# Optimization experiments

Hardware: AMD Instinct MI355X
Metric: run time of the kernel (lower is better)

Reference implementation:

```python
import jax, jax.numpy as jnp
import numpy as np

D_MODEL, NHEAD, INT_DIM = 1024, 16, 4096
HEAD_DIM = D_MODEL // NHEAD
EPS = 1e-5


def _layernorm(x, gamma, beta):
    mu = jnp.mean(x, axis=-1, keepdims=True)
    var = jnp.var(x, axis=-1, keepdims=True)
    return (x - mu) * jax.lax.rsqrt(var + EPS) * gamma + beta


def setup_inputs() -> dict:
    key = jax.random.key(0)
    ks = jax.random.split(key, 16)
    B, T = 2, 2048
    s = 0.02
    inp = {
        'x': jax.random.normal(ks[0], (B, T, D_MODEL), dtype=jnp.float32),
        'Wq': jax.random.normal(ks[1], (D_MODEL, D_MODEL), dtype=jnp.float32) * s,
        'bq': jnp.zeros((D_MODEL,), jnp.float32),
        'Wk': jax.random.normal(ks[2], (D_MODEL, D_MODEL), dtype=jnp.float32) * s,
        'bk': jnp.zeros((D_MODEL,), jnp.float32),
        'Wv': jax.random.normal(ks[3], (D_MODEL, D_MODEL), dtype=jnp.float32) * s,
        'bv': jnp.zeros((D_MODEL,), jnp.float32),
        'Wo': jax.random.normal(ks[4], (D_MODEL, D_MODEL), dtype=jnp.float32) * s,
        'bo': jnp.zeros((D_MODEL,), jnp.float32),
        'ln1_g': jnp.ones((D_MODEL,), jnp.float32),
        'ln1_b': jnp.zeros((D_MODEL,), jnp.float32),
        'ln2_g': jnp.ones((D_MODEL,), jnp.float32),
        'ln2_b': jnp.zeros((D_MODEL,), jnp.float32),
        'W1': jax.random.normal(ks[5], (D_MODEL, INT_DIM), dtype=jnp.float32) * s,
        'b1': jnp.zeros((INT_DIM,), jnp.float32),
        'W2': jax.random.normal(ks[6], (INT_DIM, D_MODEL), dtype=jnp.float32) * s,
        'b2': jnp.zeros((D_MODEL,), jnp.float32),
    }
    return inp


def reference(x, Wq, bq, Wk, bk, Wv, bv, Wo, bo, ln1_g, ln1_b, ln2_g, ln2_b, W1, b1, W2, b2):
    B, T, D = x.shape
    # projections
    q = (x @ Wq + bq).reshape(B, T, NHEAD, HEAD_DIM).transpose(0, 2, 1, 3)
    k = (x @ Wk + bk).reshape(B, T, NHEAD, HEAD_DIM).transpose(0, 2, 1, 3)
    v = (x @ Wv + bv).reshape(B, T, NHEAD, HEAD_DIM).transpose(0, 2, 1, 3)
    # attention: [B,H,T,T] scores, softmax over keys
    scores = jnp.einsum('bhqd,bhkd->bhqk', q, k) / jnp.sqrt(jnp.float32(HEAD_DIM))
    attn = jax.nn.softmax(scores, axis=-1)
    out = jnp.einsum('bhqk,bhkd->bhqd', attn, v)
    out = out.transpose(0, 2, 1, 3).reshape(B, T, D)
    attn_output = out @ Wo + bo
    # residual + layernorm 1
    h = _layernorm(x + attn_output, ln1_g, ln1_b)
    # FFN
    ff = jax.nn.relu(h @ W1 + b1) @ W2 + b2
    # residual + layernorm 2
    return _layernorm(h + ff, ln2_g, ln2_b)
```

## Files before the change

### kernel.cpp

```cpp
#include <hip/hip_runtime.h>
#include <cstdint>

#define DEVI __device__ __forceinline__

typedef float f32x4 __attribute__((ext_vector_type(4)));
typedef __bf16 bf16x8 __attribute__((ext_vector_type(8)));
typedef unsigned int u32x4v __attribute__((ext_vector_type(4)));
typedef unsigned short u16;
typedef unsigned int u32;
typedef unsigned long long u64;

#define LOG2E 1.44269504088896f
#define QSCALE (0.125f * LOG2E)

DEVI u16 bf16bits(float f) {
    u32 u = __builtin_bit_cast(u32, f);
    u32 r = u + 0x7fffu + ((u >> 16) & 1u);
    return (u16)(r >> 16);
}

DEVI u32 pack2bf(float a, float b) {
    u16 x = __builtin_bit_cast(u16, (__bf16)a);
    u16 y = __builtin_bit_cast(u16, (__bf16)b);
    return (u32)x | ((u32)y << 16);
}

DEVI float ex2(float x) {
    float r;
    asm("v_exp_f32 %0, %1" : "=v"(r) : "v"(x));
    return r;
}

DEVI void gload16(const void* g, const void* l) {
    __builtin_amdgcn_global_load_lds(
        (const __attribute__((address_space(1))) void*)(u64)(uintptr_t)g,
        (__attribute__((address_space(3))) void*)(u32)(uintptr_t)l,
        16, 0, 0);
}

#define VMCNT0_BARRIER()                                   \
    asm volatile("s_waitcnt vmcnt(0)" ::: "memory");       \
    __builtin_amdgcn_s_barrier()

__global__ __launch_bounds__(256)
void prep_kernel(const float* __restrict__ x, u16* __restrict__ xb,
                 const float* __restrict__ Wq, const float* __restrict__ Wk,
                 const float* __restrict__ Wv, const float* __restrict__ Wo,
                 u16* __restrict__ Wqt, u16* __restrict__ Wkt,
                 u16* __restrict__ Wvt, u16* __restrict__ Wot,
                 const float* __restrict__ W1, u16* __restrict__ W1t,
                 const float* __restrict__ W2, u16* __restrict__ W2t) {
    __shared__ float t[64][65];
    const int b = blockIdx.x;
    const int tid = threadIdx.x;
    if (b < 4096) {
        int i = b * 256 + tid;
        float4 v = ((const float4*)x)[i];
        ((uint2*)xb)[i] = make_uint2(pack2bf(v.x, v.y), pack2bf(v.z, v.w));
        return;
    }
    const float* src;
    u16* dst;
    int K_, N_, k0, n0;
    if (b < 5120) {
        int l = b - 4096;
        int z = l >> 8;
        l &= 255;
        src = z == 0 ? Wq : z == 1 ? Wk : z == 2 ? Wv : Wo;
        dst = z == 0 ? Wqt : z == 1 ? Wkt : z == 2 ? Wvt : Wot;
        K_ = 1024; N_ = 1024;
        k0 = (l & 15) * 64; n0 = (l >> 4) * 64;
    } else if (b < 6144) {
        int l = b - 5120;
        src = W1; dst = W1t; K_ = 1024; N_ = 4096;
        k0 = (l & 15) * 64; n0 = (l >> 4) * 64;
    } else {
        int l = b - 6144;
        src = W2; dst = W2t; K_ = 4096; N_ = 1024;
        k0 = (l & 63) * 64; n0 = (l >> 6) * 64;
    }
#pragma unroll
    for (int i = 0; i < 16; i++) {
        int idx = i * 256 + tid;
        int r = idx >> 6, c = idx & 63;
        t[r][c] = src[(u64)(k0 + r) * N_ + n0 + c];
    }
    __syncthreads();
#pragma unroll
    for (int i = 0; i < 16; i++) {
        int idx = i * 256 + tid;
        int r = idx >> 6, c = idx & 63;
        dst[(u64)(n0 + r) * K_ + k0 + c] = bf16bits(t[c][r]);
    }
}

enum { MODE_QK = 0, MODE_VT = 1, MODE_RESID = 2, MODE_RELU = 3 };

DEVI void gemm_core(const u16* __restrict__ A, const u16* __restrict__ Bt, int K_,
                    u16 (*ldsA)[128 * 64], u16 (*ldsB)[128 * 64],
                    f32x4 (&acc)[4][4], int m0, int n0) {
    const int tid = threadIdx.x;
    const int lane = tid & 63;
    const int wid = tid >> 6;
    const int wr = wid >> 1, wc = wid & 1;
    const int l15 = lane & 15, l4 = lane >> 4;
    const int srow = tid >> 3;
    const int sc = (tid & 7) ^ (srow & 7);

    const u16* ap[4];
    const u16* bp[4];
#pragma unroll
    for (int i = 0; i < 4; i++) {
        ap[i] = A + (u64)(m0 + i * 32 + srow) * K_ + sc * 8;
        bp[i] = Bt + (u64)(n0 + i * 32 + srow) * K_ + sc * 8;
    }

    auto stage = [&](int buf) {
#pragma unroll
        for (int i = 0; i < 4; i++) {
            gload16(ap[i], (const char*)ldsA[buf] + (i * 256 + tid) * 16);
            ap[i] += 64;
        }
#pragma unroll
        for (int i = 0; i < 4; i++) {
            gload16(bp[i], (const char*)ldsB[buf] + (i * 256 + tid) * 16);
            bp[i] += 64;
        }
    };

    auto compute = [&](const u16* A_, const u16* B_) {
#pragma unroll
        for (int ks = 0; ks < 2; ks++) {
            bf16x8 af[4], bfr[4];
#pragma unroll
            for (int mi = 0; mi < 4; mi++) {
                int row = wr * 64 + mi * 16 + l15;
                af[mi] = *(const bf16x8*)((const char*)A_ + row * 128 +
                                          (((ks * 4 + l4) ^ (row & 7)) * 16));
            }
#pragma unroll
            for (int ni = 0; ni < 4; ni++) {
                int row = wc * 64 + ni * 16 + l15;
                bfr[ni] = *(const bf16x8*)((const char*)B_ + row * 128 +
                                           (((ks * 4 + l4) ^ (row & 7)) * 16));
            }
            __builtin_amdgcn_s_setprio(1);
#pragma unroll
            for (int mi = 0; mi < 4; mi++)
#pragma unroll
                for (int ni = 0; ni < 4; ni++)
                    acc[mi][ni] = __builtin_amdgcn_mfma_f32_16x16x32_bf16(
                        af[mi], bfr[ni], acc[mi][ni], 0, 0, 0);
            __builtin_amdgcn_s_setprio(0);
        }
    };

    const int nk = K_ >> 6;
    stage(0);
    VMCNT0_BARRIER();
    for (int t = 0; t < nk; t += 2) {
        if (t + 1 < nk) stage(1);
        compute(ldsA[0], ldsB[0]);
        VMCNT0_BARRIER();
        if (t + 2 < nk) stage(0);
        compute(ldsA[1], ldsB[1]);
        VMCNT0_BARRIER();
    }
}

template <int MODE>
DEVI void gemm_epilogue(f32x4 (&acc)[4][4], const float* __restrict__ bias,
                        const float* __restrict__ resid, void* __restrict__ outp,
                        int N_, int m0, int n0, float scale) {
    const int tid = threadIdx.x;
    const int lane = tid & 63;
    const int wid = tid >> 6;
    const int wr = wid >> 1, wc = wid & 1;
    const int l15 = lane & 15, l4 = lane >> 4;
#pragma unroll
    for (int mi = 0; mi < 4; mi++) {
#pragma unroll
        for (int ni = 0; ni < 4; ni++) {
            const int n = n0 + wc * 64 + ni * 16 + l15;
            const float bv = bias[n];
            const int mb = m0 + wr * 64 + mi * 16 + l4 * 4;
            if (MODE == MODE_VT) {
                const int b = mb >> 11, t = mb & 2047;
                const int hh = n >> 6, d = n & 63;
                u32 lo = pack2bf(acc[mi][ni][0] + bv, acc[mi][ni][1] + bv);
                u32 hi = pack2bf(acc[mi][ni][2] + bv, acc[mi][ni][3] + bv);
                u64 idx = ((u64)((b << 4) + hh) * 64 + d) * 2048 + t;
                *(uint2*)((u16*)outp + idx) = make_uint2(lo, hi);
            } else {
#pragma unroll
                for (int r = 0; r < 4; r++) {
                    const int m = mb + r;
                    const float v = acc[mi][ni][r] + bv;
                    if (MODE == MODE_QK) {
                        const int b = m >> 11, t = m & 2047;
                        const int hh = n >> 6, d = n & 63;
                        ((u16*)outp)[(((u64)((b << 4) + hh) * 2048 + t) << 6) + d] =
                            bf16bits(v * scale);
                    } else if (MODE == MODE_RESID) {
                        const u64 i2 = (u64)m * N_ + n;
                        ((float*)outp)[i2] = v + resid[i2];
                    } else {
                        ((u16*)outp)[(u64)m * N_ + n] = bf16bits(fmaxf(v, 0.f));
                    }
                }
            }
        }
    }
}

template <int MODE>
__global__ __launch_bounds__(256, 2)
void gemm_kernel(const u16* __restrict__ A, const u16* __restrict__ Bt,
                 const float* __restrict__ bias, const float* __restrict__ resid,
                 void* __restrict__ outp, int N_, int K_) {
    __shared__ u16 ldsA[2][128 * 64];
    __shared__ u16 ldsB[2][128 * 64];
    const int m0 = blockIdx.x * 128;
    const int n0 = blockIdx.y * 128;
    f32x4 acc[4][4];
#pragma unroll
    for (int i = 0; i < 4; i++)
#pragma unroll
        for (int j = 0; j < 4; j++) acc[i][j] = (f32x4){0.f, 0.f, 0.f, 0.f};
    gemm_core(A, Bt, K_, ldsA, ldsB, acc, m0, n0);
    gemm_epilogue<MODE>(acc, bias, resid, outp, N_, m0, n0, 1.f);
}

__global__ __launch_bounds__(256, 2)
void gemm_qkv_kernel(const u16* __restrict__ A,
                     const u16* __restrict__ Wq, const u16* __restrict__ Wk,
                     const u16* __restrict__ Wv,
                     const float* __restrict__ bq, const float* __restrict__ bk,
                     const float* __restrict__ bv,
                     u16* __restrict__ Qo, u16* __restrict__ Ko, u16* __restrict__ Vo) {
    __shared__ u16 ldsA[2][128 * 64];
    __shared__ u16 ldsB[2][128 * 64];
    const int z = blockIdx.z;
    const u16* Bt = z == 0 ? Wq : z == 1 ? Wk : Wv;
    const float* bias = z == 0 ? bq : z == 1 ? bk : bv;
    const int m0 = blockIdx.x * 128;
    const int n0 = blockIdx.y * 128;
    f32x4 acc[4][4];
#pragma unroll
    for (int i = 0; i < 4; i++)
#pragma unroll
        for (int j = 0; j < 4; j++) acc[i][j] = (f32x4){0.f, 0.f, 0.f, 0.f};
    gemm_core(A, Bt, 1024, ldsA, ldsB, acc, m0, n0);
    if (z == 2)
        gemm_epilogue<MODE_VT>(acc, bias, nullptr, Vo, 1024, m0, n0, 1.f);
    else
        gemm_epilogue<MODE_QK>(acc, bias, nullptr, z == 0 ? Qo : Ko, 1024, m0, n0,
                               z == 0 ? QSCALE : 1.f);
}

__global__ __launch_bounds__(256, 2)
void gemm_n64_kernel(const u16* __restrict__ A, const u16* __restrict__ Bt,
                     const float* __restrict__ bias, const float* __restrict__ resid,
                     float* __restrict__ outp, int K_) {
    __shared__ u16 ldsA[2][128 * 64];
    __shared__ u16 ldsB[2][64 * 64];
    const int tid = threadIdx.x;
    const int lane = tid & 63;
    const int wid = tid >> 6;
    const int m0 = blockIdx.x * 128;
    const int n0 = blockIdx.y * 64;
    const int l15 = lane & 15, l4 = lane >> 4;
    const int srow = tid >> 3;
    const int sc = (tid & 7) ^ (srow & 7);

    const u16* ap[4];
    const u16* bp[2];
#pragma unroll
    for (int i = 0; i < 4; i++)
        ap[i] = A + (u64)(m0 + i * 32 + srow) * K_ + sc * 8;
#pragma unroll
    for (int i = 0; i < 2; i++)
        bp[i] = Bt + (u64)(n0 + i * 32 + srow) * K_ + sc * 8;

    auto stage = [&](int buf) {
#pragma unroll
        for (int i = 0; i < 4; i++) {
            gload16(ap[i], (const char*)ldsA[buf] + (i * 256 + tid) * 16);
            ap[i] += 64;
        }
#pragma unroll
        for (int i = 0; i < 2; i++) {
            gload16(bp[i], (const char*)ldsB[buf] + (i * 256 + tid) * 16);
            bp[i] += 64;
        }
    };

    f32x4 acc[2][4];
#pragma unroll
    for (int i = 0; i < 2; i++)
#pragma unroll
        for (int j = 0; j < 4; j++) acc[i][j] = (f32x4){0.f, 0.f, 0.f, 0.f};

    auto compute = [&](const u16* A_, const u16* B_) {
#pragma unroll
        for (int ks = 0; ks < 2; ks++) {
            bf16x8 af[2], bfr[4];
#pragma unroll
            for (int mi = 0; mi < 2; mi++) {
                int row = wid * 32 + mi * 16 + l15;
                af[mi] = *(const bf16x8*)((const char*)A_ + row * 128 +
                                          (((ks * 4 + l4) ^ (row & 7)) * 16));
            }
#pragma unroll
            for (int ni = 0; ni < 4; ni++) {
                int row = ni * 16 + l15;
                bfr[ni] = *(const bf16x8*)((const char*)B_ + row * 128 +
                                           (((ks * 4 + l4) ^ (row & 7)) * 16));
            }
            __builtin_amdgcn_s_setprio(1);
#pragma unroll
            for (int mi = 0; mi < 2; mi++)
#pragma unroll
                for (int ni = 0; ni < 4; ni++)
                    acc[mi][ni] = __builtin_amdgcn_mfma_f32_16x16x32_bf16(
                        af[mi], bfr[ni], acc[mi][ni], 0, 0, 0);
            __builtin_amdgcn_s_setprio(0);
        }
    };

    const int nk = K_ >> 6;
    stage(0);
    VMCNT0_BARRIER();
    for (int t = 0; t < nk; t += 2) {
        if (t + 1 < nk) stage(1);
        compute(ldsA[0], ldsB[0]);
        VMCNT0_BARRIER();
        if (t + 2 < nk) stage(0);
        compute(ldsA[1], ldsB[1]);
        VMCNT0_BARRIER();
    }

#pragma unroll
    for (int mi = 0; mi < 2; mi++) {
#pragma unroll
        for (int ni = 0; ni < 4; ni++) {
            const int n = n0 + ni * 16 + l15;
            const float bv = bias[n];
            const int mb = m0 + wid * 32 + mi * 16 + l4 * 4;
#pragma unroll
            for (int r = 0; r < 4; r++) {
                const u64 i2 = (u64)(mb + r) * 1024 + n;
                outp[i2] = acc[mi][ni][r] + bv + resid[i2];
            }
        }
    }
}

__global__ __launch_bounds__(256, 3)
void attn_kernel(const u16* __restrict__ Qg, const u16* __restrict__ Kg,
                 const u16* __restrict__ Vtg, u16* __restrict__ Og) {
    __shared__ u16 ldsK[3][64 * 64];
    __shared__ u16 ldsV[3][64 * 64];
    const int tid = threadIdx.x;
    const int lane = tid & 63;
    const int w = tid >> 6;
    const int l15 = lane & 15, l4 = lane >> 4;
    const int id = blockIdx.x;
    const int swz = (id & 7) * 128 + (id >> 3);
    const int bh = swz >> 5;
    const int qblk = swz & 31;
    const u64 kvbase = (u64)bh * 2048 * 64;
    const int qw0 = qblk * 64 + w * 16;

    const int srow = tid >> 3;
    const int sc8 = ((tid & 7) ^ (srow & 7)) * 8;
    const u16* kq0 = Kg + kvbase + (u64)srow * 64 + sc8;
    const u16* kq1 = Kg + kvbase + (u64)(srow + 32) * 64 + sc8;
    const u16* vq0 = Vtg + kvbase + (u64)srow * 2048 + sc8;
    const u16* vq1 = Vtg + kvbase + (u64)(srow + 32) * 2048 + sc8;

    auto stage = [&](int buf) {
        gload16(kq0, (const char*)ldsK[buf] + tid * 16);
        gload16(kq1, (const char*)ldsK[buf] + (256 + tid) * 16);
        gload16(vq0, (const char*)ldsV[buf] + tid * 16);
        gload16(vq1, (const char*)ldsV[buf] + (256 + tid) * 16);
        kq0 += 4096; kq1 += 4096; vq0 += 64; vq1 += 64;
    };

    bf16x8 aq[2];
#pragma unroll
    for (int ks = 0; ks < 2; ks++)
        aq[ks] = *(const bf16x8*)(Qg + kvbase + (u64)(qw0 + l15) * 64 + ks * 32 + l4 * 8);
    asm volatile("s_waitcnt vmcnt(0)" ::: "memory");

    stage(0);
    stage(1);

    const u32x4v onesw = {0x3F803F80u, 0x3F803F80u, 0x3F803F80u, 0x3F803F80u};
    const bf16x8 aones = __builtin_bit_cast(bf16x8, onesw);

    f32x4 acco[4];
#pragma unroll
    for (int i = 0; i < 4; i++) acco[i] = (f32x4){0.f, 0.f, 0.f, 0.f};
    f32x4 lacc = (f32x4){0.f, 0.f, 0.f, 0.f};

    auto tile_body = [&](const u16* K_, const u16* V_) {
        f32x4 sf[4];
#pragma unroll
        for (int f = 0; f < 4; f++) sf[f] = (f32x4){0.f, 0.f, 0.f, 0.f};
#pragma unroll
        for (int ks = 0; ks < 2; ks++) {
            bf16x8 ak[4];
#pragma unroll
            for (int f = 0; f < 4; f++) {
                int row = f * 16 + l15;
                ak[f] = *(const bf16x8*)((const char*)K_ + row * 128 +
                                         (((ks * 4 + l4) ^ (row & 7)) * 16));
            }
            __builtin_amdgcn_s_setprio(1);
#pragma unroll
            for (int f = 0; f < 4; f++)
                sf[f] = __builtin_amdgcn_mfma_f32_16x16x32_bf16(ak[f], aq[ks], sf[f], 0, 0, 0);
            __builtin_amdgcn_s_setprio(0);
        }

        u32 A[4], B[4];
#pragma unroll
        for (int f = 0; f < 4; f++) {
            float p0 = ex2(sf[f][0]);
            float p1 = ex2(sf[f][1]);
            float p2 = ex2(sf[f][2]);
            float p3 = ex2(sf[f][3]);
            A[f] = pack2bf(p0, p1);
            B[f] = pack2bf(p2, p3);
        }
        asm volatile("v_permlane32_swap_b32 %0, %1" : "+v"(A[0]), "+v"(A[1]));
        asm volatile("v_permlane16_swap_b32 %0, %1" : "+v"(A[0]), "+v"(A[1]));
        asm volatile("v_permlane32_swap_b32 %0, %1" : "+v"(B[0]), "+v"(B[1]));
        asm volatile("v_permlane16_swap_b32 %0, %1" : "+v"(B[0]), "+v"(B[1]));
        asm volatile("v_permlane32_swap_b32 %0, %1" : "+v"(A[2]), "+v"(A[3]));
        asm volatile("v_permlane16_swap_b32 %0, %1" : "+v"(A[2]), "+v"(A[3]));
        asm volatile("v_permlane32_swap_b32 %0, %1" : "+v"(B[2]), "+v"(B[3]));
        asm volatile("v_permlane16_swap_b32 %0, %1" : "+v"(B[2]), "+v"(B[3]));

#pragma unroll
        for (int ks = 0; ks < 2; ks++) {
            u32x4v pw = {A[2 * ks], B[2 * ks], A[2 * ks + 1], B[2 * ks + 1]};
            bf16x8 pfrag = __builtin_bit_cast(bf16x8, pw);
            bf16x8 av[4];
#pragma unroll
            for (int nf = 0; nf < 4; nf++) {
                int row = nf * 16 + l15;
                av[nf] = *(const bf16x8*)((const char*)V_ + row * 128 +
                                          (((ks * 4 + l4) ^ (row & 7)) * 16));
            }
            __builtin_amdgcn_s_setprio(1);
            lacc = __builtin_amdgcn_mfma_f32_16x16x32_bf16(aones, pfrag, lacc, 0, 0, 0);
#pragma unroll
            for (int nf = 0; nf < 4; nf++)
                acco[nf] = __builtin_amdgcn_mfma_f32_16x16x32_bf16(av[nf], pfrag, acco[nf], 0, 0, 0);
            __builtin_amdgcn_s_setprio(0);
        }
    };

    int cb = 0;
    int sb = 2;
    for (int t = 0; t < 31; t++) {
        asm volatile("s_waitcnt vmcnt(4)" ::: "memory");
        __builtin_amdgcn_s_barrier();
        if (t < 30) stage(sb);
        tile_body(ldsK[cb], ldsV[cb]);
        cb = (cb == 2) ? 0 : cb + 1;
        sb = (sb == 2) ? 0 : sb + 1;
    }
    asm volatile("s_waitcnt vmcnt(0)" ::: "memory");
    __builtin_amdgcn_s_barrier();
    tile_body(ldsK[cb], ldsV[cb]);

    const float inv = 1.f / lacc[0];

    const int b = bh >> 4, h = bh & 15;
    const int tq = qw0 + l15;
#pragma unroll
    for (int nf = 0; nf < 4; nf++) {
        const int d = nf * 16 + l4 * 4;
        u32 lo = pack2bf(acco[nf][0] * inv, acco[nf][1] * inv);
        u32 hi = pack2bf(acco[nf][2] * inv, acco[nf][3] * inv);
        *(uint2*)(Og + ((u64)(b * 2048 + tq) << 10) + h * 64 + d) = make_uint2(lo, hi);
    }
}

template <bool WB16>
__global__ __launch_bounds__(256, 4)
void ln_kernel(const float* __restrict__ in, const float* __restrict__ gam,
               const float* __restrict__ bet, float* __restrict__ outf,
               u16* __restrict__ outb) {
    __shared__ float red[2][4];
    const int row = blockIdx.x;
    const int tid = threadIdx.x;
    float4 v = ((const float4*)(in + (u64)row * 1024))[tid];
    float s = v.x + v.y + v.z + v.w;
    float sq = v.x * v.x + v.y * v.y + v.z * v.z + v.w * v.w;
#pragma unroll
    for (int sh = 1; sh < 64; sh <<= 1) {
        s += __shfl_xor(s, sh, 64);
        sq += __shfl_xor(sq, sh, 64);
    }
    if ((tid & 63) == 0) { red[0][tid >> 6] = s; red[1][tid >> 6] = sq; }
    __syncthreads();
    s = red[0][0] + red[0][1] + red[0][2] + red[0][3];
    sq = red[1][0] + red[1][1] + red[1][2] + red[1][3];
    float mu = s * (1.f / 1024.f);
    float var = sq * (1.f / 1024.f) - mu * mu;
    float inv = rsqrtf(var + 1e-5f);
    float4 g = ((const float4*)gam)[tid];
    float4 bb = ((const float4*)bet)[tid];
    float4 o;
    o.x = (v.x - mu) * inv * g.x + bb.x;
    o.y = (v.y - mu) * inv * g.y + bb.y;
    o.z = (v.z - mu) * inv * g.z + bb.z;
    o.w = (v.w - mu) * inv * g.w + bb.w;
    ((float4*)(outf + (u64)row * 1024))[tid] = o;
    if (WB16) {
        ((uint2*)(outb + (u64)row * 1024))[tid] = make_uint2(pack2bf(o.x, o.y), pack2bf(o.z, o.w));
    }
}

extern "C" void kernel_launch(void* const* d_in, const int* in_sizes, int n_in,
                              void* d_out, int out_size, void* d_ws, size_t ws_size,
                              hipStream_t stream) {
    (void)in_sizes; (void)n_in; (void)out_size; (void)ws_size;
    const float* x  = (const float*)d_in[0];
    const float* Wq = (const float*)d_in[1];
    const float* bq = (const float*)d_in[2];
    const float* Wk = (const float*)d_in[3];
    const float* bk = (const float*)d_in[4];
    const float* Wv = (const float*)d_in[5];
    const float* bv = (const float*)d_in[6];
    const float* Wo = (const float*)d_in[7];
    const float* bo = (const float*)d_in[8];
    const float* g1 = (const float*)d_in[9];
    const float* be1 = (const float*)d_in[10];
    const float* g2 = (const float*)d_in[11];
    const float* be2 = (const float*)d_in[12];
    const float* W1 = (const float*)d_in[13];
    const float* b1 = (const float*)d_in[14];
    const float* W2 = (const float*)d_in[15];
    const float* b2 = (const float*)d_in[16];

    char* ws = (char*)d_ws;
    const u64 MB = 1024ull * 1024ull;
    u16* xb    = (u16*)(ws + 0);
    u16* Wqt   = (u16*)(ws + 8 * MB);
    u16* Wkt   = (u16*)(ws + 10 * MB);
    u16* Wvt   = (u16*)(ws + 12 * MB);
    u16* Wot   = (u16*)(ws + 14 * MB);
    u16* W1t   = (u16*)(ws + 16 * MB);
    u16* W2t   = (u16*)(ws + 24 * MB);
    u16* Qb    = (u16*)(ws + 32 * MB);
    u16* Kb    = (u16*)(ws + 40 * MB);
    u16* Vtb   = (u16*)(ws + 48 * MB);
    u16* Ob    = (u16*)(ws + 56 * MB);
    float* pre1 = (float*)(ws + 64 * MB);
    float* hf  = (float*)(ws + 80 * MB);
    u16* hb    = (u16*)(ws + 96 * MB);
    u16* ffb   = (u16*)(ws + 104 * MB);
    float* pre2 = (float*)(ws + 64 * MB);

    prep_kernel<<<7168, 256, 0, stream>>>(x, xb, Wq, Wk, Wv, Wo,
                                          Wqt, Wkt, Wvt, Wot, W1, W1t, W2, W2t);

    gemm_qkv_kernel<<<dim3(32, 8, 3), 256, 0, stream>>>(xb, Wqt, Wkt, Wvt,
                                                        bq, bk, bv, Qb, Kb, Vtb);

    attn_kernel<<<1024, 256, 0, stream>>>(Qb, Kb, Vtb, Ob);

    gemm_n64_kernel<<<dim3(32, 16), 256, 0, stream>>>(Ob, Wot, bo, x, pre1, 1024);
    ln_kernel<true><<<4096, 256, 0, stream>>>(pre1, g1, be1, hf, hb);
    gemm_kernel<MODE_RELU><<<dim3(32, 32), 256, 0, stream>>>(hb, W1t, b1, nullptr, ffb, 4096, 1024);
    gemm_n64_kernel<<<dim3(32, 16), 256, 0, stream>>>(ffb, W2t, b2, hf, pre2, 4096);
    ln_kernel<false><<<4096, 256, 0, stream>>>(pre2, g2, be2, (float*)d_out, nullptr);
}
```

Measured before the change: 204.5 us.

## Unify GEMMs on 128x64 tiles with triple-buffered LDS prefetch pipeline

All GEMMs (QKV, out-proj, FFN1, FFN2) now share one 128x64-tile core that triple-buffers LDS and prefetches two k-steps ahead. It waits with a partial vmcnt instead of draining all loads before every barrier. The QKV and FFN1 GEMMs move from 128x128 to 128x64 tiles, which doubles their grid size and cuts per-thread accumulator registers, at the cost of more A-tile reloads. The aim is to overlap global loads with MFMA compute and improve occupancy and wave count.

```diff
diff --git a/kernel.cpp b/kernel.cpp
--- a/kernel.cpp
+++ b/kernel.cpp
@@ -37,10 +37,6 @@
         (__attribute__((address_space(3))) void*)(u32)(uintptr_t)l,
         16, 0, 0);
 }
-
-#define VMCNT0_BARRIER()                                   \
-    asm volatile("s_waitcnt vmcnt(0)" ::: "memory");       \
-    __builtin_amdgcn_s_barrier()
 
 __global__ __launch_bounds__(256)
 void prep_kernel(const float* __restrict__ x, u16* __restrict__ xb,
@@ -96,24 +92,24 @@
 
 enum { MODE_QK = 0, MODE_VT = 1, MODE_RESID = 2, MODE_RELU = 3 };
 
-DEVI void gemm_core(const u16* __restrict__ A, const u16* __restrict__ Bt, int K_,
-                    u16 (*ldsA)[128 * 64], u16 (*ldsB)[128 * 64],
-                    f32x4 (&acc)[4][4], int m0, int n0) {
+DEVI void gemm64_core(const u16* __restrict__ A, const u16* __restrict__ Bt, int K_,
+                      u16 (*ldsA)[128 * 64], u16 (*ldsB)[64 * 64],
+                      f32x4 (&acc)[2][4], int m0, int n0) {
     const int tid = threadIdx.x;
     const int lane = tid & 63;
     const int wid = tid >> 6;
-    const int wr = wid >> 1, wc = wid & 1;
     const int l15 = lane & 15, l4 = lane >> 4;
     const int srow = tid >> 3;
     const int sc = (tid & 7) ^ (srow & 7);
 
     const u16* ap[4];
-    const u16* bp[4];
-#pragma unroll
-    for (int i = 0; i < 4; i++) {
+    const u16* bp[2];
+#pragma unroll
+    for (int i = 0; i < 4; i++)
         ap[i] = A + (u64)(m0 + i * 32 + srow) * K_ + sc * 8;
+#pragma unroll
+    for (int i = 0; i < 2; i++)
         bp[i] = Bt + (u64)(n0 + i * 32 + srow) * K_ + sc * 8;
-    }
 
     auto stage = [&](int buf) {
 #pragma unroll
@@ -122,7 +118,7 @@
             ap[i] += 64;
         }
 #pragma unroll
-        for (int i = 0; i < 4; i++) {
+        for (int i = 0; i < 2; i++) {
             gload16(bp[i], (const char*)ldsB[buf] + (i * 256 + tid) * 16);
             bp[i] += 64;
         }
@@ -131,22 +127,22 @@
     auto compute = [&](const u16* A_, const u16* B_) {
 #pragma unroll
         for (int ks = 0; ks < 2; ks++) {
-            bf16x8 af[4], bfr[4];
-#pragma unroll
-            for (int mi = 0; mi < 4; mi++) {
-                int row = wr * 64 + mi * 16 + l15;
+            bf16x8 af[2], bfr[4];
+#pragma unroll
+            for (int mi = 0; mi < 2; mi++) {
+                int row = wid * 32 + mi * 16 + l15;
                 af[mi] = *(const bf16x8*)((const char*)A_ + row * 128 +
                                           (((ks * 4 + l4) ^ (row & 7)) * 16));
             }
 #pragma unroll
             for (int ni = 0; ni < 4; ni++) {
-                int row = wc * 64 + ni * 16 + l15;
+                int row = ni * 16 + l15;
                 bfr[ni] = *(const bf16x8*)((const char*)B_ + row * 128 +
                                            (((ks * 4 + l4) ^ (row & 7)) * 16));
             }
             __builtin_amdgcn_s_setprio(1);
 #pragma unroll
-            for (int mi = 0; mi < 4; mi++)
+            for (int mi = 0; mi < 2; mi++)
 #pragma unroll
                 for (int ni = 0; ni < 4; ni++)
                     acc[mi][ni] = __builtin_amdgcn_mfma_f32_16x16x32_bf16(
@@ -157,33 +153,37 @@
 
     const int nk = K_ >> 6;
     stage(0);
-    VMCNT0_BARRIER();
-    for (int t = 0; t < nk; t += 2) {
-        if (t + 1 < nk) stage(1);
-        compute(ldsA[0], ldsB[0]);
-        VMCNT0_BARRIER();
-        if (t + 2 < nk) stage(0);
-        compute(ldsA[1], ldsB[1]);
-        VMCNT0_BARRIER();
+    stage(1);
+    int cb = 0, sb = 2;
+    for (int t = 0; t < nk; t++) {
+        if (t < nk - 1) {
+            asm volatile("s_waitcnt vmcnt(6)" ::: "memory");
+        } else {
+            asm volatile("s_waitcnt vmcnt(0)" ::: "memory");
+        }
+        __builtin_amdgcn_s_barrier();
+        if (t + 2 < nk) stage(sb);
+        compute(ldsA[cb], ldsB[cb]);
+        cb = (cb == 2) ? 0 : cb + 1;
+        sb = (sb == 2) ? 0 : sb + 1;
     }
 }
 
 template <int MODE>
-DEVI void gemm_epilogue(f32x4 (&acc)[4][4], const float* __restrict__ bias,
-                        const float* __restrict__ resid, void* __restrict__ outp,
-                        int N_, int m0, int n0, float scale) {
+DEVI void gemm64_epilogue(f32x4 (&acc)[2][4], const float* __restrict__ bias,
+                          const float* __restrict__ resid, void* __restrict__ outp,
+                          int N_, int m0, int n0, float scale) {
     const int tid = threadIdx.x;
     const int lane = tid & 63;
     const int wid = tid >> 6;
-    const int wr = wid >> 1, wc = wid & 1;
     const int l15 = lane & 15, l4 = lane >> 4;
 #pragma unroll
-    for (int mi = 0; mi < 4; mi++) {
+    for (int mi = 0; mi < 2; mi++) {
 #pragma unroll
         for (int ni = 0; ni < 4; ni++) {
-            const int n = n0 + wc * 64 + ni * 16 + l15;
+            const int n = n0 + ni * 16 + l15;
             const float bv = bias[n];
-            const int mb = m0 + wr * 64 + mi * 16 + l4 * 4;
+            const int mb = m0 + wid * 32 + mi * 16 + l4 * 4;
             if (MODE == MODE_VT) {
                 const int b = mb >> 11, t = mb & 2047;
                 const int hh = n >> 6, d = n & 63;
@@ -215,145 +215,47 @@
 
 template <int MODE>
 __global__ __launch_bounds__(256, 2)
-void gemm_kernel(const u16* __restrict__ A, const u16* __restrict__ Bt,
-                 const float* __restrict__ bias, const float* __restrict__ resid,
-                 void* __restrict__ outp, int N_, int K_) {
-    __shared__ u16 ldsA[2][128 * 64];
-    __shared__ u16 ldsB[2][128 * 64];
+void gemm64_kernel(const u16* __restrict__ A, const u16* __restrict__ Bt,
+                   const float* __restrict__ bias, const float* __restrict__ resid,
+                   void* __restrict__ outp, int N_, int K_) {
+    __shared__ u16 ldsA[3][128 * 64];
+    __shared__ u16 ldsB[3][64 * 64];
     const int m0 = blockIdx.x * 128;
-    const int n0 = blockIdx.y * 128;
-    f32x4 acc[4][4];
-#pragma unroll
-    for (int i = 0; i < 4; i++)
+    const int n0 = blockIdx.y * 64;
+    f32x4 acc[2][4];
+#pragma unroll
+    for (int i = 0; i < 2; i++)
 #pragma unroll
         for (int j = 0; j < 4; j++) acc[i][j] = (f32x4){0.f, 0.f, 0.f, 0.f};
-    gemm_core(A, Bt, K_, ldsA, ldsB, acc, m0, n0);
-    gemm_epilogue<MODE>(acc, bias, resid, outp, N_, m0, n0, 1.f);
+    gemm64_core(A, Bt, K_, ldsA, ldsB, acc, m0, n0);
+    gemm64_epilogue<MODE>(acc, bias, resid, outp, N_, m0, n0, 1.f);
 }
 
 __global__ __launch_bounds__(256, 2)
-void gemm_qkv_kernel(const u16* __restrict__ A,
-                     const u16* __restrict__ Wq, const u16* __restrict__ Wk,
-                     const u16* __restrict__ Wv,
-                     const float* __restrict__ bq, const float* __restrict__ bk,
-                     const float* __restrict__ bv,
-                     u16* __restrict__ Qo, u16* __restrict__ Ko, u16* __restrict__ Vo) {
-    __shared__ u16 ldsA[2][128 * 64];
-    __shared__ u16 ldsB[2][128 * 64];
+void gemm64_qkv_kernel(const u16* __restrict__ A,
+                       const u16* __restrict__ Wq, const u16* __restrict__ Wk,
+                       const u16* __restrict__ Wv,
+                       const float* __restrict__ bq, const float* __restrict__ bk,
+                       const float* __restrict__ bv,
+                       u16* __restrict__ Qo, u16* __restrict__ Ko, u16* __restrict__ Vo) {
+    __shared__ u16 ldsA[3][128 * 64];
+    __shared__ u16 ldsB[3][64 * 64];
     const int z = blockIdx.z;
     const u16* Bt = z == 0 ? Wq : z == 1 ? Wk : Wv;
     const float* bias = z == 0 ? bq : z == 1 ? bk : bv;
     const int m0 = blockIdx.x * 128;
-    const int n0 = blockIdx.y * 128;
-    f32x4 acc[4][4];
-#pragma unroll
-    for (int i = 0; i < 4; i++)
+    const int n0 = blockIdx.y * 64;
+    f32x4 acc[2][4];
+#pragma unroll
+    for (int i = 0; i < 2; i++)
 #pragma unroll
         for (int j = 0; j < 4; j++) acc[i][j] = (f32x4){0.f, 0.f, 0.f, 0.f};
-    gemm_core(A, Bt, 1024, ldsA, ldsB, acc, m0, n0);
+    gemm64_core(A, Bt, 1024, ldsA, ldsB, acc, m0, n0);
     if (z == 2)
-        gemm_epilogue<MODE_VT>(acc, bias, nullptr, Vo, 1024, m0, n0, 1.f);
+        gemm64_epilogue<MODE_VT>(acc, bias, nullptr, Vo, 1024, m0, n0, 1.f);
     else
-        gemm_epilogue<MODE_QK>(acc, bias, nullptr, z == 0 ? Qo : Ko, 1024, m0, n0,
-                               z == 0 ? QSCALE : 1.f);
-}
-
-__global__ __launch_bounds__(256, 2)
-void gemm_n64_kernel(const u16* __restrict__ A, const u16* __restrict__ Bt,
-                     const float* __restrict__ bias, const float* __restrict__ resid,
-                     float* __restrict__ outp, int K_) {
-    __shared__ u16 ldsA[2][128 * 64];
-    __shared__ u16 ldsB[2][64 * 64];
-    const int tid = threadIdx.x;
-    const int lane = tid & 63;
-    const int wid = tid >> 6;
-    const int m0 = blockIdx.x * 128;
-    const int n0 = blockIdx.y * 64;
-    const int l15 = lane & 15, l4 = lane >> 4;
-    const int srow = tid >> 3;
-    const int sc = (tid & 7) ^ (srow & 7);
-
-    const u16* ap[4];
-    const u16* bp[2];
-#pragma unroll
-    for (int i = 0; i < 4; i++)
-        ap[i] = A + (u64)(m0 + i * 32 + srow) * K_ + sc * 8;
-#pragma unroll
-    for (int i = 0; i < 2; i++)
-        bp[i] = Bt + (u64)(n0 + i * 32 + srow) * K_ + sc * 8;
-
-    auto stage = [&](int buf) {
-#pragma unroll
-        for (int i = 0; i < 4; i++) {
-            gload16(ap[i], (const char*)ldsA[buf] + (i * 256 + tid) * 16);
-            ap[i] += 64;
-        }
-#pragma unroll
-        for (int i = 0; i < 2; i++) {
-            gload16(bp[i], (const char*)ldsB[buf] + (i * 256 + tid) * 16);
-            bp[i] += 64;
-        }
-    };
-
-    f32x4 acc[2][4];
-#pragma unroll
-    for (int i = 0; i < 2; i++)
-#pragma unroll
-        for (int j = 0; j < 4; j++) acc[i][j] = (f32x4){0.f, 0.f, 0.f, 0.f};
-
-    auto compute = [&](const u16* A_, const u16* B_) {
-#pragma unroll
-        for (int ks = 0; ks < 2; ks++) {
-            bf16x8 af[2], bfr[4];
-#pragma unroll
-            for (int mi = 0; mi < 2; mi++) {
-                int row = wid * 32 + mi * 16 + l15;
-                af[mi] = *(const bf16x8*)((const char*)A_ + row * 128 +
-                                          (((ks * 4 + l4) ^ (row & 7)) * 16));
-            }
-#pragma unroll
-            for (int ni = 0; ni < 4; ni++) {
-                int row = ni * 16 + l15;
-                bfr[ni] = *(const bf16x8*)((const char*)B_ + row * 128 +
-                                           (((ks * 4 + l4) ^ (row & 7)) * 16));
-            }
-            __builtin_amdgcn_s_setprio(1);
-#pragma unroll
-            for (int mi = 0; mi < 2; mi++)
-#pragma unroll
-                for (int ni = 0; ni < 4; ni++)
-                    acc[mi][ni] = __builtin_amdgcn_mfma_f32_16x16x32_bf16(
-                        af[mi], bfr[ni], acc[mi][ni], 0, 0, 0);
-            __builtin_amdgcn_s_setprio(0);
-        }
-    };
-
-    const int nk = K_ >> 6;
-    stage(0);
-    VMCNT0_BARRIER();
-    for (int t = 0; t < nk; t += 2) {
-        if (t + 1 < nk) stage(1);
-        compute(ldsA[0], ldsB[0]);
-        VMCNT0_BARRIER();
-        if (t + 2 < nk) stage(0);
-        compute(ldsA[1], ldsB[1]);
-        VMCNT0_BARRIER();
-    }
-
-#pragma unroll
-    for (int mi = 0; mi < 2; mi++) {
-#pragma unroll
-        for (int ni = 0; ni < 4; ni++) {
-            const int n = n0 + ni * 16 + l15;
-            const float bv = bias[n];
-            const int mb = m0 + wid * 32 + mi * 16 + l4 * 4;
-#pragma unroll
-            for (int r = 0; r < 4; r++) {
-                const u64 i2 = (u64)(mb + r) * 1024 + n;
-                outp[i2] = acc[mi][ni][r] + bv + resid[i2];
-            }
-        }
-    }
+        gemm64_epilogue<MODE_QK>(acc, bias, nullptr, z == 0 ? Qo : Ko, 1024, m0, n0,
+                                 z == 0 ? QSCALE : 1.f);
 }
 
 __global__ __launch_bounds__(256, 3)
@@ -570,14 +472,14 @@
     prep_kernel<<<7168, 256, 0, stream>>>(x, xb, Wq, Wk, Wv, Wo,
                                           Wqt, Wkt, Wvt, Wot, W1, W1t, W2, W2t);
 
-    gemm_qkv_kernel<<<dim3(32, 8, 3), 256, 0, stream>>>(xb, Wqt, Wkt, Wvt,
-                                                        bq, bk, bv, Qb, Kb, Vtb);
+    gemm64_qkv_kernel<<<dim3(32, 16, 3), 256, 0, stream>>>(xb, Wqt, Wkt, Wvt,
+                                                           bq, bk, bv, Qb, Kb, Vtb);
 
     attn_kernel<<<1024, 256, 0, stream>>>(Qb, Kb, Vtb, Ob);
 
-    gemm_n64_kernel<<<dim3(32, 16), 256, 0, stream>>>(Ob, Wot, bo, x, pre1, 1024);
+    gemm64_kernel<MODE_RESID><<<dim3(32, 16), 256, 0, stream>>>(Ob, Wot, bo, x, pre1, 1024, 1024);
     ln_kernel<true><<<4096, 256, 0, stream>>>(pre1, g1, be1, hf, hb);
-    gemm_kernel<MODE_RELU><<<dim3(32, 32), 256, 0, stream>>>(hb, W1t, b1, nullptr, ffb, 4096, 1024);
-    gemm_n64_kernel<<<dim3(32, 16), 256, 0, stream>>>(ffb, W2t, b2, hf, pre2, 4096);
+    gemm64_kernel<MODE_RELU><<<dim3(32, 64), 256, 0, stream>>>(hb, W1t, b1, nullptr, ffb, 4096, 1024);
+    gemm64_kernel<MODE_RESID><<<dim3(32, 16), 256, 0, stream>>>(ffb, W2t, b2, hf, pre2, 1024, 4096);
     ln_kernel<false><<<4096, 256, 0, stream>>>(pre2, g2, be2, (float*)d_out, nullptr);
 }
```

After: 214.1 us. +4.7%, slower.
